# Kernel tuning notes

Measured on AMD Instinct MI355X. Metric: run time of the kernel, lower is better.

The kernel has to match this reference:

```python
import jax, jax.numpy as jnp
import numpy as np

OBS, ACT, EMB, HID, NQ = 512, 32, 512, 512, 32
B = 32768


def setup_inputs() -> dict:
    key = jax.random.key(0)
    ks = jax.random.split(key, 12)
    s_in = 1.0 / np.sqrt(OBS + ACT)
    s_emb = 1.0 / np.sqrt(EMB)
    s_hid = 1.0 / np.sqrt(HID)
    return {
        "observation": jax.random.normal(ks[0], (B, OBS), jnp.float32),
        "prev_action": jax.random.normal(ks[1], (B, ACT), jnp.float32),
        "hidden_state": jax.random.normal(ks[2], (HID,), jnp.float32),
        "cell_state": jax.random.normal(ks[3], (HID,), jnp.float32),
        "W1": jax.random.uniform(ks[4], (EMB, OBS + ACT), jnp.float32, -s_in, s_in),
        "b1": jax.random.uniform(ks[5], (EMB,), jnp.float32, -s_in, s_in),
        "W_ih": jax.random.uniform(ks[6], (4 * HID, EMB), jnp.float32, -s_hid, s_hid),
        "b_ih": jax.random.uniform(ks[7], (4 * HID,), jnp.float32, -s_hid, s_hid),
        "W_hh": jax.random.uniform(ks[8], (4 * HID, HID), jnp.float32, -s_hid, s_hid),
        "b_hh": jax.random.uniform(ks[9], (4 * HID,), jnp.float32, -s_hid, s_hid),
        "W2": jax.random.uniform(ks[10], (NQ, HID), jnp.float32, -s_hid, s_hid),
        "b2": jax.random.uniform(ks[11], (NQ,), jnp.float32, -s_hid, s_hid),
    }


def reference(observation, prev_action, hidden_state, cell_state,
              W1, b1, W_ih, b_ih, W_hh, b_hh, W2, b2):
    # MLP1: Linear + ReLU over concat(obs, prev_action)  -> [B, EMB]
    x = jnp.concatenate([observation, prev_action], axis=-1)
    x = jax.nn.relu(x @ W1.T + b1)

    # Original torch code loops LSTMCell over batch, but reuses the SAME
    # (hidden_state, cell_state) every iteration -> fully batchable.
    # gates: [B, 4H]; h contribution is identical for all rows (broadcast).
    gates = x @ W_ih.T + b_ih + (hidden_state @ W_hh.T + b_hh)
    i, f, g, o = jnp.split(gates, 4, axis=-1)  # torch LSTMCell gate order
    i = jax.nn.sigmoid(i)
    f = jax.nn.sigmoid(f)
    g = jnp.tanh(g)
    o = jax.nn.sigmoid(o)
    c_new = f * cell_state + i * g          # [B, HID]
    h_new = o * jnp.tanh(c_new)             # [B, HID]

    q_values = h_new @ W2.T + b2             # [B, NQ]
    # torch returns last loop iteration's (h, c)
    return q_values, h_new[-1], c_new[-1]
```

## Files before the change

kernel.cpp:

```cpp
#include <hip/hip_runtime.h>
#include <stdint.h>

#define DEVINL __device__ __forceinline__

typedef __attribute__((ext_vector_type(8))) __bf16 bf16x8;
typedef __attribute__((ext_vector_type(4))) float f32x4;
typedef __attribute__((ext_vector_type(16))) float f32x16;
typedef __attribute__((ext_vector_type(4))) int i32x4;
typedef __attribute__((ext_vector_type(8))) int i32x8;

DEVINL unsigned short f2bf(float f) {
  union { float f; unsigned int u; } v; v.f = f;
  unsigned int u = v.u;
  return (unsigned short)((u + 0x7fffu + ((u >> 16) & 1u)) >> 16);
}

DEVINL unsigned int cvtpk_bf16(float lo, float hi) {
  unsigned int r;
  asm("v_cvt_pk_bf16_f32 %0, %1, %2" : "=v"(r) : "v"(lo), "v"(hi));
  return r;
}

DEVINL unsigned char f2fp8(float f) {
  return (unsigned char)(__builtin_amdgcn_cvt_pk_fp8_f32(f, f, 0, false) & 0xff);
}

DEVINL float sigm(float x) { return __builtin_amdgcn_rcpf(1.f + __expf(-x)); }
DEVINL float tanh_(float x) {
  return 1.f - 2.f * __builtin_amdgcn_rcpf(1.f + __expf(2.f * x));
}

DEVINL size_t opt_off(int row, int k) {
  return (size_t)((row >> 5) * 8 + (k >> 6)) * 2048 + ((k >> 4) & 1) * 1024 +
         ((k >> 5) & 1) * 512 + (row & 31) * 16 + (k & 15);
}

#define GLD_LDS16(gptr, lptr)                                                  \
  __builtin_amdgcn_global_load_lds(                                            \
      (__attribute__((address_space(1))) void*)(gptr),                         \
      (__attribute__((address_space(3))) void*)(lptr), 16, 0, 0)

#define KT_BAR asm volatile("s_waitcnt vmcnt(0) lgkmcnt(0)\n\ts_barrier" ::: "memory")

DEVINL int swz_col(int c) { return ((c & 3) ^ ((c >> 3) & 3)) * 8; }

__global__ void prep_all(const float* __restrict__ W1, const float* __restrict__ Wih,
                         const float* __restrict__ W2, const float* __restrict__ Whh,
                         const float* __restrict__ hid, const float* __restrict__ bhh,
                         const float* __restrict__ bih,
                         unsigned short* __restrict__ W1b,
                         unsigned char* __restrict__ Wih8, unsigned short* __restrict__ W2b,
                         float* __restrict__ hvec) {
  const int bid = blockIdx.x, tid = threadIdx.x;
  if (bid < 1312) {
    const int i = bid * 256 + tid;
    if (i < 69632) {
      float4 f = *(const float4*)(W1 + (size_t)i * 4);
      unsigned short u[4] = {f2bf(f.x), f2bf(f.y), f2bf(f.z), f2bf(f.w)};
      *(uint2*)(W1b + (size_t)i * 4) = *(uint2*)u;
    } else if (i < 69632 + 262144) {
      const int off = i - 69632;
      const int row = off >> 7, col0 = (off & 127) * 4;
      float4 f = *(const float4*)(Wih + (size_t)off * 4);
      int pk = __builtin_amdgcn_cvt_pk_fp8_f32(f.x * 16.f, f.y * 16.f, 0, false);
      pk = __builtin_amdgcn_cvt_pk_fp8_f32(f.z * 16.f, f.w * 16.f, pk, true);
      *(unsigned int*)(Wih8 + opt_off(row, col0)) = (unsigned int)pk;
    } else {
      const int off = i - 331776;
      float4 f = *(const float4*)(W2 + (size_t)off * 4);
      unsigned short u[4] = {f2bf(f.x), f2bf(f.y), f2bf(f.z), f2bf(f.w)};
      *(uint2*)(W2b + (size_t)off * 4) = *(uint2*)u;
    }
  } else {
    const int j = (bid - 1312) * 4 + (tid >> 6);
    const int lane = tid & 63;
    const float* w = Whh + (size_t)j * 512;
    float s = 0.f;
    for (int k = lane; k < 512; k += 64) s += w[k] * hid[k];
    for (int off = 32; off; off >>= 1) s += __shfl_down(s, off, 64);
    if (lane == 0) hvec[j] = s + bhh[j] + bih[j];
  }
}

__global__ __launch_bounds__(256, 2) void gemm1_relu(
    const float* __restrict__ obs,
    const float* __restrict__ act,
    const unsigned short* __restrict__ W1b,
    const float* __restrict__ b1,
    unsigned char* __restrict__ X8) {
  constexpr int KT = 17;
  __shared__ __align__(16) unsigned short As[2][4096];
  __shared__ __align__(16) unsigned short Bs[2][4096];
  const int tid = threadIdx.x, wave = tid >> 6, lane = tid & 63;
  const int id = blockIdx.x, xcd = id & 7, slot = id >> 3;
  const int m0 = (xcd * 32 + (slot >> 2)) * 128;
  const int n0 = (slot & 3) * 128;
  const int wr = (wave >> 1) * 64, wc = (wave & 1) * 64;
  f32x4 acc[4][4] = {};

  const int c0 = tid, c1 = tid + 256;
  const int r0 = c0 >> 2, r1 = c1 >> 2;
  const int sw0 = swz_col(c0), sw1 = swz_col(c1);
  const float* pObs0 = obs + (size_t)(m0 + r0) * 512 + sw0;
  const float* pObs1 = obs + (size_t)(m0 + r1) * 512 + sw1;
  const float* pAct0 = act + (size_t)(m0 + r0) * 32 + sw0;
  const float* pAct1 = act + (size_t)(m0 + r1) * 32 + sw1;
  const unsigned short* pB0 = W1b + (size_t)(n0 + r0) * 544 + sw0;
  const unsigned short* pB1 = W1b + (size_t)(n0 + r1) * 544 + sw1;
  const int fr = lane & 15, q = lane >> 4;
  const int koff = (q ^ ((fr >> 1) & 3)) * 8;

  float4 fA00, fA01, fA10, fA11;

#define LOADA(kt)                                                              \
  do {                                                                         \
    const float* s0_ = ((kt) < 16) ? (pObs0 + (kt) * 32) : pAct0;              \
    const float* s1_ = ((kt) < 16) ? (pObs1 + (kt) * 32) : pAct1;              \
    fA00 = *(const float4*)s0_; fA01 = *(const float4*)(s0_ + 4);              \
    fA10 = *(const float4*)s1_; fA11 = *(const float4*)(s1_ + 4);              \
  } while (0)

#define GLDB(buf)                                                              \
  do {                                                                         \
    GLD_LDS16(pB0, &Bs[(buf)][wave * 512]);                                    \
    GLD_LDS16(pB1, &Bs[(buf)][2048 + wave * 512]);                             \
    pB0 += 32; pB1 += 32;                                                      \
  } while (0)

#define CVTWR(buf)                                                             \
  do {                                                                         \
    unsigned int w0_[4] = {cvtpk_bf16(fA00.x, fA00.y), cvtpk_bf16(fA00.z, fA00.w), \
                           cvtpk_bf16(fA01.x, fA01.y), cvtpk_bf16(fA01.z, fA01.w)}; \
    *(uint4*)&As[(buf)][c0 * 8] = *(uint4*)w0_;                                \
    unsigned int w1_[4] = {cvtpk_bf16(fA10.x, fA10.y), cvtpk_bf16(fA10.z, fA10.w), \
                           cvtpk_bf16(fA11.x, fA11.y), cvtpk_bf16(fA11.z, fA11.w)}; \
    *(uint4*)&As[(buf)][c1 * 8] = *(uint4*)w1_;                                \
  } while (0)

  LOADA(0);
  GLDB(0);
  CVTWR(0);
  KT_BAR;

#pragma unroll
  for (int kt = 0; kt < KT; ++kt) {
    if (kt < 16) { LOADA(kt + 1); GLDB((kt + 1) & 1); }
    const unsigned short* as = As[kt & 1];
    const unsigned short* bs = Bs[kt & 1];
    bf16x8 a[4], b[4];
#pragma unroll
    for (int i = 0; i < 4; ++i) a[i] = *(const bf16x8*)&as[(wr + i * 16 + fr) * 32 + koff];
#pragma unroll
    for (int j = 0; j < 4; ++j) b[j] = *(const bf16x8*)&bs[(wc + j * 16 + fr) * 32 + koff];
#pragma unroll
    for (int i = 0; i < 4; ++i)
#pragma unroll
      for (int j = 0; j < 4; ++j)
        acc[i][j] = __builtin_amdgcn_mfma_f32_16x16x32_bf16(a[i], b[j], acc[i][j], 0, 0, 0);
    if (kt < 16) {
      CVTWR((kt + 1) & 1);
      KT_BAR;
    }
  }
#undef LOADA
#undef GLDB
#undef CVTWR

  const int rbase = q * 4, cn = fr;
#pragma unroll
  for (int i = 0; i < 4; ++i)
#pragma unroll
    for (int j = 0; j < 4; ++j) {
      const int gn = n0 + wc + j * 16 + cn;
      const float bias = b1[gn];
#pragma unroll
      for (int r = 0; r < 4; ++r) {
        const int gm = m0 + wr + i * 16 + rbase + r;
        float v = acc[i][j][r] + bias;
        v = v > 0.f ? v : 0.f;
        X8[opt_off(gm, gn)] = f2fp8(v * 8.f);
      }
    }
}

__global__ __launch_bounds__(256, 2) void gemm2_lstm(
    const unsigned char* __restrict__ X8,
    const unsigned char* __restrict__ Wih8,
    const float* __restrict__ hvec,
    const float* __restrict__ cell,
    unsigned short* __restrict__ H,
    float* __restrict__ hlast,
    float* __restrict__ clast) {
  __shared__ __align__(16) unsigned char Bs[4 * 16384];
  const int tid = threadIdx.x, wave = tid >> 6, lane = tid & 63;
  const int id = blockIdx.x, xcd = id & 7, slot = id >> 3;
  const int m0 = (xcd * 16 + (slot >> 4)) * 256;
  const int n0 = (slot & 15) * 32;
  const int r31 = lane & 31, g2 = lane >> 5;
  const int voff = g2 * 512 + r31 * 16;

  {
    const unsigned char* bsrc =
        Wih8 + (size_t)(wave * 16 + (n0 >> 5)) * 16384 + lane * 16;
#pragma unroll
    for (int s = 0; s < 16; ++s)
      GLD_LDS16(bsrc + s * 1024, &Bs[wave * 16384 + s * 1024]);
  }

  const unsigned char* pa = X8 + (size_t)((m0 >> 5) + wave * 2) * 16384 + voff;
  i32x8 Aa[3], Ab[3];
#define LDA(buf, kt)                                                           \
  do {                                                                         \
    i32x4 lo0 = *(const i32x4*)(pa + (kt) * 2048);                             \
    i32x4 hi0 = *(const i32x4*)(pa + (kt) * 2048 + 1024);                      \
    Aa[buf] = __builtin_shufflevector(lo0, hi0, 0, 1, 2, 3, 4, 5, 6, 7);       \
    i32x4 lo1 = *(const i32x4*)(pa + 16384 + (kt) * 2048);                     \
    i32x4 hi1 = *(const i32x4*)(pa + 16384 + (kt) * 2048 + 1024);              \
    Ab[buf] = __builtin_shufflevector(lo1, hi1, 0, 1, 2, 3, 4, 5, 6, 7);       \
  } while (0)

#define MFMA_MX(acc_, a_, b_)                                                  \
  acc_ = __builtin_amdgcn_mfma_scale_f32_32x32x64_f8f6f4(                      \
      a_, b_, acc_, 0, 0, 0, 0x7f7f7f7f, 0, 0x7f7f7f7f)

  LDA(0, 0);
  LDA(1, 1);
  __syncthreads();

  f32x16 acc00 = {}, acc01 = {}, acc02 = {}, acc03 = {};
  f32x16 acc10 = {}, acc11 = {}, acc12 = {}, acc13 = {};

#pragma unroll
  for (int kt = 0; kt < 8; ++kt) {
    const int cur = kt % 3, nx = (kt + 2) % 3;
    if (kt < 6) LDA(nx, kt + 2);
    i32x8 B0, B1, B2, B3;
    {
      const unsigned char* bb = &Bs[kt * 2048 + lane * 16];
      i32x4 l0 = *(const i32x4*)(bb);
      i32x4 h0 = *(const i32x4*)(bb + 1024);
      i32x4 l1 = *(const i32x4*)(bb + 16384);
      i32x4 h1 = *(const i32x4*)(bb + 16384 + 1024);
      i32x4 l2 = *(const i32x4*)(bb + 32768);
      i32x4 h2 = *(const i32x4*)(bb + 32768 + 1024);
      i32x4 l3 = *(const i32x4*)(bb + 49152);
      i32x4 h3 = *(const i32x4*)(bb + 49152 + 1024);
      B0 = __builtin_shufflevector(l0, h0, 0, 1, 2, 3, 4, 5, 6, 7);
      B1 = __builtin_shufflevector(l1, h1, 0, 1, 2, 3, 4, 5, 6, 7);
      B2 = __builtin_shufflevector(l2, h2, 0, 1, 2, 3, 4, 5, 6, 7);
      B3 = __builtin_shufflevector(l3, h3, 0, 1, 2, 3, 4, 5, 6, 7);
    }
    MFMA_MX(acc00, Aa[cur], B0); MFMA_MX(acc01, Aa[cur], B1);
    MFMA_MX(acc02, Aa[cur], B2); MFMA_MX(acc03, Aa[cur], B3);
    MFMA_MX(acc10, Ab[cur], B0); MFMA_MX(acc11, Ab[cur], B1);
    MFMA_MX(acc12, Ab[cur], B2); MFMA_MX(acc13, Ab[cur], B3);
  }
#undef LDA
#undef MFMA_MX

  const int gn = n0 + r31;
  const float hv_i = hvec[gn];
  const float hv_f = hvec[gn + 512];
  const float hv_g = hvec[gn + 1024];
  const float hv_o = hvec[gn + 1536];
  const float cprev = cell[gn];
  constexpr float S = 1.f / 128.f;

#define EPILOG(F, ai, af, ag, ao)                                              \
  _Pragma("unroll")                                                            \
  for (int rg = 0; rg < 4; ++rg) {                                             \
    _Pragma("unroll")                                                          \
    for (int rr = 0; rr < 4; ++rr) {                                           \
      const int reg = rg * 4 + rr;                                             \
      const int gm = m0 + wave * 64 + (F) * 32 + rr + rg * 8 + g2 * 4;         \
      float si = sigm(ai[reg] * S + hv_i);                                     \
      float sf = sigm(af[reg] * S + hv_f);                                     \
      float tg = tanh_(ag[reg] * S + hv_g);                                    \
      float so = sigm(ao[reg] * S + hv_o);                                     \
      float cnew = sf * cprev + si * tg;                                       \
      float hnew = so * tanh_(cnew);                                           \
      H[(size_t)gm * 512 + gn] = f2bf(hnew);                                   \
      if (gm == 32767) { hlast[gn] = hnew; clast[gn] = cnew; }                 \
    }                                                                          \
  }

  EPILOG(0, acc00, acc01, acc02, acc03)
  EPILOG(1, acc10, acc11, acc12, acc13)
#undef EPILOG
}

__global__ __launch_bounds__(256, 2) void gemm3(
    const unsigned short* __restrict__ H,
    const unsigned short* __restrict__ W2b,
    const float* __restrict__ b2,
    float* __restrict__ Q) {
  constexpr int LDW = 520;
  __shared__ __align__(16) unsigned short Ws[32 * LDW];
  const int tid = threadIdx.x, wave = tid >> 6, lane = tid & 63;
  const int id = blockIdx.x;
  const int m0 = ((id & 7) * 64 + (id >> 3)) * 64 + wave * 16;
  for (int c = tid; c < 2048; c += 256) {
    const int row = c >> 6, col8 = c & 63;
    *(uint4*)&Ws[row * LDW + col8 * 8] = *(const uint4*)(W2b + row * 512 + col8 * 8);
  }
  __syncthreads();

  const int fr = lane & 15, q = lane >> 4;
  f32x4 acc[2] = {};
  const unsigned short* pH = H + (size_t)(m0 + fr) * 512 + q * 8;
#pragma unroll
  for (int kt = 0; kt < 16; ++kt) {
    const int k0 = kt * 32;
    bf16x8 a  = *(const bf16x8*)(pH + k0);
    bf16x8 b0 = *(const bf16x8*)&Ws[fr * LDW + k0 + q * 8];
    bf16x8 b1 = *(const bf16x8*)&Ws[(16 + fr) * LDW + k0 + q * 8];
    acc[0] = __builtin_amdgcn_mfma_f32_16x16x32_bf16(a, b0, acc[0], 0, 0, 0);
    acc[1] = __builtin_amdgcn_mfma_f32_16x16x32_bf16(a, b1, acc[1], 0, 0, 0);
  }

  const int rbase = q * 4;
#pragma unroll
  for (int j = 0; j < 2; ++j) {
    const int gn = j * 16 + fr;
    const float bias = b2[gn];
#pragma unroll
    for (int r = 0; r < 4; ++r) {
      const int gm = m0 + rbase + r;
      Q[(size_t)gm * 32 + gn] = acc[j][r] + bias;
    }
  }
}

extern "C" void kernel_launch(void* const* d_in, const int* in_sizes, int n_in,
                              void* d_out, int out_size, void* d_ws, size_t ws_size,
                              hipStream_t stream) {
  const float* obs  = (const float*)d_in[0];
  const float* act  = (const float*)d_in[1];
  const float* hid  = (const float*)d_in[2];
  const float* cell = (const float*)d_in[3];
  const float* W1   = (const float*)d_in[4];
  const float* b1   = (const float*)d_in[5];
  const float* Wih  = (const float*)d_in[6];
  const float* bih  = (const float*)d_in[7];
  const float* Whh  = (const float*)d_in[8];
  const float* bhh  = (const float*)d_in[9];
  const float* W2   = (const float*)d_in[10];
  const float* b2   = (const float*)d_in[11];
  float* out = (float*)d_out;

  char* ws = (char*)d_ws;
  unsigned short* H    = (unsigned short*)(ws);
  unsigned char*  X8   = (unsigned char*)(ws + 35651584);
  unsigned short* W1b  = (unsigned short*)(ws + 52428800);
  unsigned char*  Wih8 = (unsigned char*)(ws + 52985856);
  unsigned short* W2b  = (unsigned short*)(ws + 54034432);
  float*          hvec = (float*)(ws + 54067200);

  prep_all<<<1824, 256, 0, stream>>>(W1, Wih, W2, Whh, hid, bhh, bih,
                                     W1b, Wih8, W2b, hvec);
  gemm1_relu<<<1024, 256, 0, stream>>>(obs, act, W1b, b1, X8);
  gemm2_lstm<<<2048, 256, 0, stream>>>(X8, Wih8, hvec, cell, H,
                                       out + 32768 * 32,
                                       out + 32768 * 32 + 512);
  gemm3<<<512, 256, 0, stream>>>(H, W2b, b2, out);
}
```

Measured before the change: 219.7 us.

## Load GEMM1 MFMA fragments directly from global memory, dropping LDS staging

The first GEMM no longer stages A (fp32 obs/act converted to bf16) and B (bf16 W1) tiles through shared memory with barriers. Each wave now loads its own MFMA fragments straight from global memory into registers, double-buffered two K-steps ahead, and converts A to bf16 in registers. This removes LDS writes, reads and block barriers. In exchange, each A row is loaded by both column-waves and each B row by both row-waves, so global/L2 traffic roughly doubles, and register pressure rises under launch_bounds(256,2).

```diff
diff --git a/kernel.cpp b/kernel.cpp
--- a/kernel.cpp
+++ b/kernel.cpp
@@ -39,10 +39,6 @@
   __builtin_amdgcn_global_load_lds(                                            \
       (__attribute__((address_space(1))) void*)(gptr),                         \
       (__attribute__((address_space(3))) void*)(lptr), 16, 0, 0)
-
-#define KT_BAR asm volatile("s_waitcnt vmcnt(0) lgkmcnt(0)\n\ts_barrier" ::: "memory")
-
-DEVINL int swz_col(int c) { return ((c & 3) ^ ((c >> 3) & 3)) * 8; }
 
 __global__ void prep_all(const float* __restrict__ W1, const float* __restrict__ Wih,
                          const float* __restrict__ W2, const float* __restrict__ Whh,
@@ -88,83 +84,61 @@
     const unsigned short* __restrict__ W1b,
     const float* __restrict__ b1,
     unsigned char* __restrict__ X8) {
-  constexpr int KT = 17;
-  __shared__ __align__(16) unsigned short As[2][4096];
-  __shared__ __align__(16) unsigned short Bs[2][4096];
   const int tid = threadIdx.x, wave = tid >> 6, lane = tid & 63;
   const int id = blockIdx.x, xcd = id & 7, slot = id >> 3;
   const int m0 = (xcd * 32 + (slot >> 2)) * 128;
   const int n0 = (slot & 3) * 128;
   const int wr = (wave >> 1) * 64, wc = (wave & 1) * 64;
+  const int fr = lane & 15, q = lane >> 4;
   f32x4 acc[4][4] = {};
 
-  const int c0 = tid, c1 = tid + 256;
-  const int r0 = c0 >> 2, r1 = c1 >> 2;
-  const int sw0 = swz_col(c0), sw1 = swz_col(c1);
-  const float* pObs0 = obs + (size_t)(m0 + r0) * 512 + sw0;
-  const float* pObs1 = obs + (size_t)(m0 + r1) * 512 + sw1;
-  const float* pAct0 = act + (size_t)(m0 + r0) * 32 + sw0;
-  const float* pAct1 = act + (size_t)(m0 + r1) * 32 + sw1;
-  const unsigned short* pB0 = W1b + (size_t)(n0 + r0) * 544 + sw0;
-  const unsigned short* pB1 = W1b + (size_t)(n0 + r1) * 544 + sw1;
-  const int fr = lane & 15, q = lane >> 4;
-  const int koff = (q ^ ((fr >> 1) & 3)) * 8;
-
-  float4 fA00, fA01, fA10, fA11;
-
-#define LOADA(kt)                                                              \
+  const float* aro[4];
+  const float* ara[4];
+  const unsigned short* brw[4];
+#pragma unroll
+  for (int i = 0; i < 4; ++i) {
+    aro[i] = obs + (size_t)(m0 + wr + i * 16 + fr) * 512 + q * 8;
+    ara[i] = act + (size_t)(m0 + wr + i * 16 + fr) * 32 + q * 8;
+    brw[i] = W1b + (size_t)(n0 + wc + i * 16 + fr) * 544 + q * 8;
+  }
+
+  float4 Af[2][4][2];
+  bf16x8 Bf[2][4];
+
+#define LOADSET(s, K)                                                          \
   do {                                                                         \
-    const float* s0_ = ((kt) < 16) ? (pObs0 + (kt) * 32) : pAct0;              \
-    const float* s1_ = ((kt) < 16) ? (pObs1 + (kt) * 32) : pAct1;              \
-    fA00 = *(const float4*)s0_; fA01 = *(const float4*)(s0_ + 4);              \
-    fA10 = *(const float4*)s1_; fA11 = *(const float4*)(s1_ + 4);              \
+    _Pragma("unroll")                                                          \
+    for (int i_ = 0; i_ < 4; ++i_) {                                           \
+      const float* p_ = ((K) < 16) ? (aro[i_] + (K) * 32) : ara[i_];           \
+      Af[s][i_][0] = *(const float4*)p_;                                       \
+      Af[s][i_][1] = *(const float4*)(p_ + 4);                                 \
+      Bf[s][i_] = *(const bf16x8*)(brw[i_] + (K) * 32);                        \
+    }                                                                          \
   } while (0)
 
-#define GLDB(buf)                                                              \
-  do {                                                                         \
-    GLD_LDS16(pB0, &Bs[(buf)][wave * 512]);                                    \
-    GLD_LDS16(pB1, &Bs[(buf)][2048 + wave * 512]);                             \
-    pB0 += 32; pB1 += 32;                                                      \
-  } while (0)
-
-#define CVTWR(buf)                                                             \
-  do {                                                                         \
-    unsigned int w0_[4] = {cvtpk_bf16(fA00.x, fA00.y), cvtpk_bf16(fA00.z, fA00.w), \
-                           cvtpk_bf16(fA01.x, fA01.y), cvtpk_bf16(fA01.z, fA01.w)}; \
-    *(uint4*)&As[(buf)][c0 * 8] = *(uint4*)w0_;                                \
-    unsigned int w1_[4] = {cvtpk_bf16(fA10.x, fA10.y), cvtpk_bf16(fA10.z, fA10.w), \
-                           cvtpk_bf16(fA11.x, fA11.y), cvtpk_bf16(fA11.z, fA11.w)}; \
-    *(uint4*)&As[(buf)][c1 * 8] = *(uint4*)w1_;                                \
-  } while (0)
-
-  LOADA(0);
-  GLDB(0);
-  CVTWR(0);
-  KT_BAR;
-
-#pragma unroll
-  for (int kt = 0; kt < KT; ++kt) {
-    if (kt < 16) { LOADA(kt + 1); GLDB((kt + 1) & 1); }
-    const unsigned short* as = As[kt & 1];
-    const unsigned short* bs = Bs[kt & 1];
-    bf16x8 a[4], b[4];
-#pragma unroll
-    for (int i = 0; i < 4; ++i) a[i] = *(const bf16x8*)&as[(wr + i * 16 + fr) * 32 + koff];
-#pragma unroll
-    for (int j = 0; j < 4; ++j) b[j] = *(const bf16x8*)&bs[(wc + j * 16 + fr) * 32 + koff];
+  LOADSET(0, 0);
+  LOADSET(1, 1);
+
+#pragma unroll
+  for (int kt = 0; kt < 17; ++kt) {
+    const int s = kt & 1;
+    bf16x8 a[4];
+#pragma unroll
+    for (int i = 0; i < 4; ++i) {
+      unsigned int w_[4] = {cvtpk_bf16(Af[s][i][0].x, Af[s][i][0].y),
+                            cvtpk_bf16(Af[s][i][0].z, Af[s][i][0].w),
+                            cvtpk_bf16(Af[s][i][1].x, Af[s][i][1].y),
+                            cvtpk_bf16(Af[s][i][1].z, Af[s][i][1].w)};
+      a[i] = *(bf16x8*)w_;
+    }
 #pragma unroll
     for (int i = 0; i < 4; ++i)
 #pragma unroll
       for (int j = 0; j < 4; ++j)
-        acc[i][j] = __builtin_amdgcn_mfma_f32_16x16x32_bf16(a[i], b[j], acc[i][j], 0, 0, 0);
-    if (kt < 16) {
-      CVTWR((kt + 1) & 1);
-      KT_BAR;
-    }
-  }
-#undef LOADA
-#undef GLDB
-#undef CVTWR
+        acc[i][j] = __builtin_amdgcn_mfma_f32_16x16x32_bf16(a[i], Bf[s][j], acc[i][j], 0, 0, 0);
+    if (kt + 2 < 17) LOADSET(s, kt + 2);
+  }
+#undef LOADSET
 
   const int rbase = q * 4, cn = fr;
 #pragma unroll
```

Result: slower. 280.9 us (+27.9%).
